# Optimization experiments

Hardware: AMD Instinct MI355X
Metric: run time of the kernel (lower is better)

## Reference

```python
import jax, jax.numpy as jnp
import numpy as np

N_NODES = 200000
N_EDGES = 4000000  # doubled (w2b + b2w), matches edge_weight param size
N_W2B = 2000000


def gcn_conv(x, W, b, src, dst, ew, n):
    # PyG GCNConv with add_self_loops=True, symmetric normalization.
    loop = jnp.arange(n)
    src_sl = jnp.concatenate([src, loop])
    dst_sl = jnp.concatenate([dst, loop])
    w_sl = jnp.concatenate([ew, jnp.ones((n,), ew.dtype)])  # self-loop weight 1
    deg = jax.ops.segment_sum(w_sl, dst_sl, num_segments=n)
    dinv = jnp.where(deg > 0, jax.lax.rsqrt(deg), 0.0)
    norm = dinv[src_sl] * w_sl * dinv[dst_sl]          # [E+N]
    xw = x @ W                                          # [N, out]
    msg = xw[src_sl] * norm[:, None]                    # [E+N, out]
    out = jax.ops.segment_sum(msg, dst_sl, num_segments=n)
    return out + b


def setup_inputs() -> dict:
    key = jax.random.key(0)
    ks = jax.random.split(key, 16)
    h1, h2, h3, h4, out = 8, 16, 32, 4, 3
    inp = 7

    def lin_init(k, fan_in, fan_out):
        bound = 1.0 / np.sqrt(fan_in)
        kw, kb = jax.random.split(k)
        W = jax.random.uniform(kw, (fan_in, fan_out), jnp.float32, -bound, bound)
        b = jax.random.uniform(kb, (fan_out,), jnp.float32, -bound, bound)
        return W, b

    x = jax.random.normal(ks[0], (N_NODES, inp), jnp.float32)
    edge_index = jax.random.randint(ks[1], (2, N_EDGES), 0, N_NODES, jnp.int64)
    w2b = jax.random.randint(ks[2], (2, N_W2B), 0, N_NODES, jnp.int64)
    edge_weight = jnp.ones((N_EDGES,), jnp.float32)  # Parameter init: ones

    W1, b1 = lin_init(ks[3], inp, h1)
    W2, b2 = lin_init(ks[4], h1, h2)
    W3, b3 = lin_init(ks[5], h2, h3)
    Wl1, bl1 = lin_init(ks[6], 2 * h3, h4)
    Wl2, bl2 = lin_init(ks[7], h4, out)

    return dict(x=x, edge_index=edge_index, w2b=w2b, edge_weight=edge_weight,
                W1=W1, b1=b1, W2=W2, b2=b2, W3=W3, b3=b3,
                Wl1=Wl1, bl1=bl1, Wl2=Wl2, bl2=bl2)


def reference(x, edge_index, w2b, edge_weight,
              W1, b1, W2, b2, W3, b3, Wl1, bl1, Wl2, bl2):
    n = x.shape[0]
    src, dst = edge_index[0], edge_index[1]
    ew = jax.nn.sigmoid(edge_weight)
    h = jax.nn.relu(gcn_conv(x, W1, b1, src, dst, ew, n))
    h = jax.nn.relu(gcn_conv(h, W2, b2, src, dst, ew, n))
    h = jax.nn.relu(gcn_conv(h, W3, b3, src, dst, ew, n))
    # fused gather-concat replacing the per-edge python loop
    concat = jnp.concatenate([h[w2b[0]], h[w2b[1]]], axis=-1)  # [E_w2b, 2*h3]
    hidden = concat @ Wl1 + bl1
    edge_pred = hidden @ Wl2 + bl2
    return edge_pred
```

## Files before the change

kernel.cpp:

```cpp
#include <hip/hip_runtime.h>
#include <hip/hip_bf16.h>
#include <hip/hip_fp16.h>


#define NB1 768
#define NPB 256
#define MAXBINS 1024
#define TILE 4096
#define QS 16384.0f
#define QINV (1.0f / 16384.0f)

typedef _Float16 h2 __attribute__((ext_vector_type(2)));
typedef _Float16 h4 __attribute__((ext_vector_type(4)));
typedef _Float16 h8 __attribute__((ext_vector_type(8)));

__device__ __forceinline__ float sigmoidf_(float x) {
    return 1.0f / (1.0f + __expf(-x));
}

__global__ void p1a_hist(const int* __restrict__ dst, int* __restrict__ bh,
                         int ne, int nbins, int chunk) {
    __shared__ int h[MAXBINS];
    for (int k = threadIdx.x; k < nbins; k += 256) h[k] = 0;
    __syncthreads();
    int base = blockIdx.x * chunk;
    int end = min(base + chunk, ne);
    for (int e = base + threadIdx.x; e < end; e += 256)
        atomicAdd(&h[dst[e] >> 8], 1);
    __syncthreads();
    for (int k = threadIdx.x; k < nbins; k += 256)
        bh[(size_t)k * NB1 + blockIdx.x] = h[k];
}

__global__ void s1_scan(int* __restrict__ bh, int* __restrict__ bintot) {
    __shared__ int sums[256];
    constexpr int W = NB1 / 256;
    int* row = bh + (size_t)blockIdx.x * NB1;
    int v[W];
    int s = 0;
#pragma unroll
    for (int j = 0; j < W; ++j) { v[j] = row[threadIdx.x * W + j]; s += v[j]; }
    sums[threadIdx.x] = s;
    __syncthreads();
    for (int o = 1; o < 256; o <<= 1) {
        int t = (threadIdx.x >= o) ? sums[threadIdx.x - o] : 0;
        __syncthreads();
        sums[threadIdx.x] += t;
        __syncthreads();
    }
    int excl = sums[threadIdx.x] - s;
#pragma unroll
    for (int j = 0; j < W; ++j) { row[threadIdx.x * W + j] = excl; excl += v[j]; }
    if (threadIdx.x == 255) bintot[blockIdx.x] = sums[255];
}

__global__ void s2_scan(const int* __restrict__ bintot, int* __restrict__ binbase,
                        int nbins, int ne) {
    __shared__ int tmp[1024];
    int tid = threadIdx.x;
    int v = (tid < nbins) ? bintot[tid] : 0;
    tmp[tid] = v;
    __syncthreads();
    for (int o = 1; o < 1024; o <<= 1) {
        int t = (tid >= o) ? tmp[tid - o] : 0;
        __syncthreads();
        tmp[tid] += t;
        __syncthreads();
    }
    if (tid < nbins) binbase[tid] = tmp[tid] - v;
    if (tid == 0) binbase[nbins] = ne;
}

__global__ void p1b_scatter(const int* __restrict__ src, const int* __restrict__ dst,
                            const float* __restrict__ ew, const int* __restrict__ bh,
                            const int* __restrict__ binbase,
                            unsigned* __restrict__ edlo, unsigned char* __restrict__ eddl,
                            int ne, int nbins, int chunk) {
    __shared__ unsigned slo[TILE];
    __shared__ unsigned shi[TILE];
    __shared__ int hist[MAXBINS];
    __shared__ int boff[MAXBINS];
    __shared__ int cur[MAXBINS];
    __shared__ int wsum[4];
    int tid = threadIdx.x;
    int lane = tid & 63, wid = tid >> 6;
    for (int k = tid; k < nbins; k += 256)
        cur[k] = binbase[k] + bh[(size_t)k * NB1 + blockIdx.x];
    int base = blockIdx.x * chunk;
    int endb = min(base + chunk, ne);
    for (int t0 = base; t0 < endb; t0 += TILE) {
        int cnt = min(TILE, endb - t0);
        for (int k = tid; k < nbins; k += 256) hist[k] = 0;
        __syncthreads();
        for (int j = tid; j < cnt; j += 256)
            atomicAdd(&hist[dst[t0 + j] >> 8], 1);
        __syncthreads();
        int w0 = tid * 4;
        int lv[4];
        int ls = 0;
#pragma unroll
        for (int j = 0; j < 4; ++j) {
            lv[j] = (w0 + j < nbins) ? hist[w0 + j] : 0;
            ls += lv[j];
        }
        int s = ls;
        for (int o = 1; o < 64; o <<= 1) {
            int t = __shfl_up(s, o, 64);
            if (lane >= o) s += t;
        }
        if (lane == 63) wsum[wid] = s;
        __syncthreads();
        int wpre = 0;
        for (int w = 0; w < wid; ++w) wpre += wsum[w];
        int excl = wpre + s - ls;
#pragma unroll
        for (int j = 0; j < 4; ++j) {
            if (w0 + j < nbins) { boff[w0 + j] = excl; excl += lv[j]; }
        }
        __syncthreads();
        for (int j = tid; j < cnt; j += 256) {
            int e = t0 + j;
            int d = dst[e];
            int b = d >> 8;
            float w = sigmoidf_(ew[e]);
            int q = (int)fminf(w * QS + 0.5f, 16383.0f);
            unsigned lo = (unsigned)src[e] | ((unsigned)q << 18);
            int p = atomicAdd(&boff[b], 1);
            slo[p] = lo;
            shi[p] = ((unsigned)b << 8) | (unsigned)(d & 255);
        }
        __syncthreads();
        for (int j = tid; j < cnt; j += 256) {
            unsigned hv = shi[j];
            int b = (int)(hv >> 8);
            int g = cur[b] + (j - (boff[b] - hist[b]));
            edlo[g] = slo[j];
            eddl[g] = (unsigned char)(hv & 255u);
        }
        __syncthreads();
        for (int k = tid; k < nbins; k += 256) cur[k] += hist[k];
        __syncthreads();
    }
}

__global__ void p2_build(const unsigned* __restrict__ edlo, const unsigned char* __restrict__ eddl,
                         const int* __restrict__ binbase, unsigned* __restrict__ edata,
                         int* __restrict__ C, float* __restrict__ dinv,
                         const float* __restrict__ x, const float* __restrict__ W1,
                         _Float16* __restrict__ g0, int n, int ne, int nbins) {
    __shared__ int cnt[NPB];
    __shared__ int curs[NPB];
    __shared__ unsigned qsum[NPB];
    __shared__ float Ws[56];
    __shared__ int wsum[4];
    if (threadIdx.x < 56) Ws[threadIdx.x] = W1[threadIdx.x];
    int b = blockIdx.x;
    int E0 = binbase[b], E1 = binbase[b + 1];
    int tid = threadIdx.x;
    int lane = tid & 63, wid = tid >> 6;
    cnt[tid] = 0;
    qsum[tid] = 0;
    __syncthreads();
    for (int k = E0 + tid; k < E1; k += 256)
        atomicAdd(&cnt[(int)eddl[k]], 1);
    __syncthreads();
    int v = cnt[tid];
    int s = v;
    for (int o = 1; o < 64; o <<= 1) {
        int t = __shfl_up(s, o, 64);
        if (lane >= o) s += t;
    }
    if (lane == 63) wsum[wid] = s;
    __syncthreads();
    int wpre = 0;
    for (int w = 0; w < wid; ++w) wpre += wsum[w];
    int excl = wpre + s - v;
    curs[tid] = E0 + excl;
    int node = b * NPB + tid;
    if (node < n) C[node] = E0 + excl;
    if (b == 0 && tid == 0) C[n] = ne;
    __syncthreads();
    for (int k = E0 + tid; k < E1; k += 256) {
        unsigned lo = edlo[k];
        int dl = (int)eddl[k];
        int pos = atomicAdd(&curs[dl], 1);
        edata[pos] = lo;
        atomicAdd(&qsum[dl], lo >> 18);
    }
    __syncthreads();
    if (node < n) {
        float dv = rsqrtf((float)qsum[tid] * QINV + 1.0f);
        dinv[node] = dv;
        float xi[7];
#pragma unroll
        for (int k = 0; k < 7; ++k) xi[k] = x[(size_t)node * 7 + k];
        h8 r;
#pragma unroll
        for (int o = 0; o < 8; ++o) {
            float acc = 0.0f;
#pragma unroll
            for (int k = 0; k < 7; ++k) acc = fmaf(xi[k], Ws[k * 8 + o], acc);
            r[o] = (_Float16)(acc * dv);
        }
        *reinterpret_cast<h8*>(g0 + (size_t)node * 8) = r;
    }
}

__global__ void gather1_kernel(const _Float16* __restrict__ g, const float* __restrict__ dinv,
                               const int* __restrict__ C, const unsigned* __restrict__ edata,
                               const float* __restrict__ b1, _Float16* __restrict__ out, int n) {
    __shared__ float bs[8];
    if (threadIdx.x < 8) bs[threadIdx.x] = b1[threadIdx.x];
    __syncthreads();
    long long t = (long long)blockIdx.x * blockDim.x + threadIdx.x;
    int i = (int)(t >> 3);
    int l8 = (int)(t & 7);
    if (i >= n) return;
    int beg = C[i], end = C[i + 1];
    float acc[8] = {0.f, 0.f, 0.f, 0.f, 0.f, 0.f, 0.f, 0.f};
    if (l8 == 0) {
        h8 r = *reinterpret_cast<const h8*>(g + (size_t)i * 8);
#pragma unroll
        for (int j = 0; j < 8; ++j) acc[j] = (float)r[j];
    }
    int k = beg + l8;
    for (; k + 8 < end; k += 16) {
        unsigned v0 = edata[k];
        unsigned v1 = edata[k + 8];
        h8 r0 = *reinterpret_cast<const h8*>(g + (size_t)(v0 & 0x3FFFFu) * 8);
        h8 r1 = *reinterpret_cast<const h8*>(g + (size_t)(v1 & 0x3FFFFu) * 8);
        float w0 = (float)(v0 >> 18) * QINV;
        float w1 = (float)(v1 >> 18) * QINV;
#pragma unroll
        for (int j = 0; j < 8; ++j) acc[j] = fmaf((float)r0[j], w0, acc[j]);
#pragma unroll
        for (int j = 0; j < 8; ++j) acc[j] = fmaf((float)r1[j], w1, acc[j]);
    }
    if (k < end) {
        unsigned v = edata[k];
        float w = (float)(v >> 18) * QINV;
        h8 r = *reinterpret_cast<const h8*>(g + (size_t)(v & 0x3FFFFu) * 8);
#pragma unroll
        for (int j = 0; j < 8; ++j) acc[j] = fmaf((float)r[j], w, acc[j]);
    }
    bool t4 = (l8 & 4) != 0, t2 = (l8 & 2) != 0, t1 = (l8 & 1) != 0;
    float s4[4];
#pragma unroll
    for (int j = 0; j < 4; ++j) {
        float keep = t4 ? acc[4 + j] : acc[j];
        float send = t4 ? acc[j] : acc[4 + j];
        s4[j] = keep + __shfl_xor(send, 4, 64);
    }
    float s2[2];
#pragma unroll
    for (int j = 0; j < 2; ++j) {
        float keep = t2 ? s4[2 + j] : s4[j];
        float send = t2 ? s4[j] : s4[2 + j];
        s2[j] = keep + __shfl_xor(send, 2, 64);
    }
    float keep = t1 ? s2[1] : s2[0];
    float send = t1 ? s2[0] : s2[1];
    float s = keep + __shfl_xor(send, 1, 64);
    float dv = dinv[i];
    out[(size_t)i * 8 + l8] = (_Float16)(dv * fmaxf(dv * s + bs[l8], 0.0f));
}

__global__ void gather2_kernel(const _Float16* __restrict__ g, const float* __restrict__ dinv,
                               const int* __restrict__ C, const unsigned* __restrict__ edata,
                               const float* __restrict__ W2, const float* __restrict__ b2,
                               _Float16* __restrict__ out, int n) {
    __shared__ float Ws[128];
    __shared__ float bs[16];
    if (threadIdx.x < 128) Ws[threadIdx.x] = W2[threadIdx.x];
    if (threadIdx.x < 16) bs[threadIdx.x] = b2[threadIdx.x];
    __syncthreads();
    long long t = (long long)blockIdx.x * blockDim.x + threadIdx.x;
    int i = (int)(t >> 3);
    int l8 = (int)(t & 7);
    if (i >= n) return;
    int beg = C[i], end = C[i + 1];
    float acc[8] = {0.f, 0.f, 0.f, 0.f, 0.f, 0.f, 0.f, 0.f};
    if (l8 == 0) {
        h8 r = *reinterpret_cast<const h8*>(g + (size_t)i * 8);
#pragma unroll
        for (int j = 0; j < 8; ++j) acc[j] = (float)r[j];
    }
    int k = beg + l8;
    for (; k + 8 < end; k += 16) {
        unsigned v0 = edata[k];
        unsigned v1 = edata[k + 8];
        h8 r0 = *reinterpret_cast<const h8*>(g + (size_t)(v0 & 0x3FFFFu) * 8);
        h8 r1 = *reinterpret_cast<const h8*>(g + (size_t)(v1 & 0x3FFFFu) * 8);
        float w0 = (float)(v0 >> 18) * QINV;
        float w1 = (float)(v1 >> 18) * QINV;
#pragma unroll
        for (int j = 0; j < 8; ++j) acc[j] = fmaf((float)r0[j], w0, acc[j]);
#pragma unroll
        for (int j = 0; j < 8; ++j) acc[j] = fmaf((float)r1[j], w1, acc[j]);
    }
    if (k < end) {
        unsigned v = edata[k];
        float w = (float)(v >> 18) * QINV;
        h8 r = *reinterpret_cast<const h8*>(g + (size_t)(v & 0x3FFFFu) * 8);
#pragma unroll
        for (int j = 0; j < 8; ++j) acc[j] = fmaf((float)r[j], w, acc[j]);
    }
#pragma unroll
    for (int j = 0; j < 8; ++j) {
        acc[j] += __shfl_xor(acc[j], 1, 64);
        acc[j] += __shfl_xor(acc[j], 2, 64);
        acc[j] += __shfl_xor(acc[j], 4, 64);
    }
    float dv = dinv[i];
    float raw[8];
#pragma unroll
    for (int j = 0; j < 8; ++j) raw[j] = acc[j] * dv;
    int o0 = l8 * 2;
    h2 o2;
#pragma unroll
    for (int jo = 0; jo < 2; ++jo) {
        int o = o0 + jo;
        float h = bs[o];
#pragma unroll
        for (int k2 = 0; k2 < 8; ++k2) h = fmaf(raw[k2], Ws[k2 * 16 + o], h);
        o2[jo] = (_Float16)(dv * fmaxf(h, 0.0f));
    }
    *reinterpret_cast<h2*>(out + (size_t)i * 16 + o0) = o2;
}

__global__ void gather3_kernel(const _Float16* __restrict__ g, const float* __restrict__ dinv,
                               const int* __restrict__ C, const unsigned* __restrict__ edata,
                               _Float16* __restrict__ raw3, int n) {
    long long t = (long long)blockIdx.x * blockDim.x + threadIdx.x;
    int i = (int)(t >> 3);
    int l8 = (int)(t & 7);
    if (i >= n) return;
    int beg = C[i], end = C[i + 1];
    float acc[16];
#pragma unroll
    for (int j = 0; j < 16; ++j) acc[j] = 0.0f;
    if (l8 == 0) {
        h8 r0 = *reinterpret_cast<const h8*>(g + (size_t)i * 16);
        h8 r1 = *reinterpret_cast<const h8*>(g + (size_t)i * 16 + 8);
#pragma unroll
        for (int j = 0; j < 8; ++j) { acc[j] = (float)r0[j]; acc[8 + j] = (float)r1[j]; }
    }
    int k = beg + l8;
    for (; k + 8 < end; k += 16) {
        unsigned v0 = edata[k];
        unsigned v1 = edata[k + 8];
        size_t i0 = (size_t)(v0 & 0x3FFFFu) * 16;
        size_t i1 = (size_t)(v1 & 0x3FFFFu) * 16;
        h8 a0 = *reinterpret_cast<const h8*>(g + i0);
        h8 a1 = *reinterpret_cast<const h8*>(g + i0 + 8);
        h8 c0 = *reinterpret_cast<const h8*>(g + i1);
        h8 c1 = *reinterpret_cast<const h8*>(g + i1 + 8);
        float w0 = (float)(v0 >> 18) * QINV;
        float w1 = (float)(v1 >> 18) * QINV;
#pragma unroll
        for (int j = 0; j < 8; ++j) acc[j] = fmaf((float)a0[j], w0, acc[j]);
#pragma unroll
        for (int j = 0; j < 8; ++j) acc[8 + j] = fmaf((float)a1[j], w0, acc[8 + j]);
#pragma unroll
        for (int j = 0; j < 8; ++j) acc[j] = fmaf((float)c0[j], w1, acc[j]);
#pragma unroll
        for (int j = 0; j < 8; ++j) acc[8 + j] = fmaf((float)c1[j], w1, acc[8 + j]);
    }
    if (k < end) {
        unsigned v = edata[k];
        size_t i0 = (size_t)(v & 0x3FFFFu) * 16;
        h8 a0 = *reinterpret_cast<const h8*>(g + i0);
        h8 a1 = *reinterpret_cast<const h8*>(g + i0 + 8);
        float w = (float)(v >> 18) * QINV;
#pragma unroll
        for (int j = 0; j < 8; ++j) acc[j] = fmaf((float)a0[j], w, acc[j]);
#pragma unroll
        for (int j = 0; j < 8; ++j) acc[8 + j] = fmaf((float)a1[j], w, acc[8 + j]);
    }
    bool t4 = (l8 & 4) != 0, t2 = (l8 & 2) != 0, t1 = (l8 & 1) != 0;
    float s8[8];
#pragma unroll
    for (int j = 0; j < 8; ++j) {
        float keep = t4 ? acc[8 + j] : acc[j];
        float send = t4 ? acc[j] : acc[8 + j];
        s8[j] = keep + __shfl_xor(send, 4, 64);
    }
    float s4[4];
#pragma unroll
    for (int j = 0; j < 4; ++j) {
        float keep = t2 ? s8[4 + j] : s8[j];
        float send = t2 ? s8[j] : s8[4 + j];
        s4[j] = keep + __shfl_xor(send, 2, 64);
    }
    float s2[2];
#pragma unroll
    for (int j = 0; j < 2; ++j) {
        float keep = t1 ? s4[2 + j] : s4[j];
        float send = t1 ? s4[j] : s4[2 + j];
        s2[j] = keep + __shfl_xor(send, 1, 64);
    }
    float dv = dinv[i];
    h2 o2;
    o2[0] = (_Float16)(s2[0] * dv);
    o2[1] = (_Float16)(s2[1] * dv);
    *reinterpret_cast<h2*>(raw3 + (size_t)i * 16 + l8 * 2) = o2;
}

__global__ void dense3_kernel(const _Float16* __restrict__ raw3,
                              const float* __restrict__ W3, const float* __restrict__ b3,
                              const float* __restrict__ Wl1, const float* __restrict__ bl1,
                              const float* __restrict__ Wl2, const float* __restrict__ bl2,
                              _Float16* __restrict__ pqh, int n) {
    __shared__ __align__(16) float WsT[512];
    __shared__ float bs[32];
    __shared__ float wfs[192];
    __shared__ float bfs[3];
    for (int t = threadIdx.x; t < 512; t += 256) {
        int k = t >> 5, o = t & 31;
        WsT[o * 16 + k] = W3[t];
    }
    if (threadIdx.x < 32) bs[threadIdx.x] = b3[threadIdx.x];
    if (threadIdx.x < 192) {
        int f = threadIdx.x / 3, j = threadIdx.x % 3;
        float a = 0.0f;
#pragma unroll
        for (int k = 0; k < 4; ++k) a = fmaf(Wl1[f * 4 + k], Wl2[k * 3 + j], a);
        wfs[threadIdx.x] = a;
    }
    if (threadIdx.x < 3) {
        float a = bl2[threadIdx.x];
#pragma unroll
        for (int k = 0; k < 4; ++k) a = fmaf(bl1[k], Wl2[k * 3 + threadIdx.x], a);
        bfs[threadIdx.x] = a;
    }
    __syncthreads();
    int i = blockIdx.x * 256 + threadIdx.x;
    if (i >= n) return;
    h8 r0 = *reinterpret_cast<const h8*>(raw3 + (size_t)i * 16);
    h8 r1 = *reinterpret_cast<const h8*>(raw3 + (size_t)i * 16 + 8);
    float raw[16];
#pragma unroll
    for (int j = 0; j < 8; ++j) { raw[j] = (float)r0[j]; raw[8 + j] = (float)r1[j]; }
    float p0 = bfs[0], p1 = bfs[1], p2 = bfs[2];
    float q0 = 0.0f, q1 = 0.0f, q2 = 0.0f;
#pragma unroll
    for (int o = 0; o < 32; ++o) {
        const float4* w4 = reinterpret_cast<const float4*>(WsT + o * 16);
        float4 wa = w4[0], wb = w4[1], wc = w4[2], wd = w4[3];
        float h = bs[o];
        h = fmaf(raw[0], wa.x, h);  h = fmaf(raw[1], wa.y, h);
        h = fmaf(raw[2], wa.z, h);  h = fmaf(raw[3], wa.w, h);
        h = fmaf(raw[4], wb.x, h);  h = fmaf(raw[5], wb.y, h);
        h = fmaf(raw[6], wb.z, h);  h = fmaf(raw[7], wb.w, h);
        h = fmaf(raw[8], wc.x, h);  h = fmaf(raw[9], wc.y, h);
        h = fmaf(raw[10], wc.z, h); h = fmaf(raw[11], wc.w, h);
        h = fmaf(raw[12], wd.x, h); h = fmaf(raw[13], wd.y, h);
        h = fmaf(raw[14], wd.z, h); h = fmaf(raw[15], wd.w, h);
        h = fmaxf(h, 0.0f);
        p0 = fmaf(h, wfs[o * 3 + 0], p0);
        p1 = fmaf(h, wfs[o * 3 + 1], p1);
        p2 = fmaf(h, wfs[o * 3 + 2], p2);
        q0 = fmaf(h, wfs[(32 + o) * 3 + 0], q0);
        q1 = fmaf(h, wfs[(32 + o) * 3 + 1], q1);
        q2 = fmaf(h, wfs[(32 + o) * 3 + 2], q2);
    }
    h8 o8;
    o8[0] = (_Float16)p0; o8[1] = (_Float16)p1; o8[2] = (_Float16)p2; o8[3] = (_Float16)0.0f;
    o8[4] = (_Float16)q0; o8[5] = (_Float16)q1; o8[6] = (_Float16)q2; o8[7] = (_Float16)0.0f;
    *reinterpret_cast<h8*>(pqh + (size_t)i * 8) = o8;
}

__global__ void head_kernel(const int* __restrict__ w2b, const _Float16* __restrict__ pqh,
                            float* __restrict__ out, int nw) {
    int e = blockIdx.x * blockDim.x + threadIdx.x;
    if (e >= nw) return;
    int a = w2b[e];
    int b = w2b[(size_t)nw + e];
    h4 P = *reinterpret_cast<const h4*>(pqh + (size_t)a * 8);
    h4 Q = *reinterpret_cast<const h4*>(pqh + (size_t)b * 8 + 4);
    out[(size_t)e * 3 + 0] = (float)P[0] + (float)Q[0];
    out[(size_t)e * 3 + 1] = (float)P[1] + (float)Q[1];
    out[(size_t)e * 3 + 2] = (float)P[2] + (float)Q[2];
}

extern "C" void kernel_launch(void* const* d_in, const int* in_sizes, int n_in,
                              void* d_out, int out_size, void* d_ws, size_t ws_size,
                              hipStream_t stream) {
    const float* x   = (const float*)d_in[0];
    const int* eidx  = (const int*)d_in[1];
    const int* w2b   = (const int*)d_in[2];
    const float* ew  = (const float*)d_in[3];
    const float* W1  = (const float*)d_in[4];
    const float* b1  = (const float*)d_in[5];
    const float* W2  = (const float*)d_in[6];
    const float* b2  = (const float*)d_in[7];
    const float* W3  = (const float*)d_in[8];
    const float* b3  = (const float*)d_in[9];
    const float* Wl1 = (const float*)d_in[10];
    const float* bl1 = (const float*)d_in[11];
    const float* Wl2 = (const float*)d_in[12];
    const float* bl2 = (const float*)d_in[13];
    float* out = (float*)d_out;

    const int n  = in_sizes[0] / 7;
    const int ne = in_sizes[1] / 2;
    const int nw = in_sizes[2] / 2;
    const int* src = eidx;
    const int* dst = eidx + ne;

    const int nbins = (n + NPB - 1) / NPB;
    const int chunk = (ne + NB1 - 1) / NB1;

    float*     ws      = (float*)d_ws;
    float*     dinv    = ws;
    int*       C       = (int*)(ws + n);
    unsigned*  edata   = (unsigned*)(ws + 2 * (size_t)n + 16);
    int*       bh      = (int*)(edata + ne);
    int*       bintot  = bh + (size_t)nbins * NB1;
    int*       binbase = bintot + MAXBINS;
    _Float16*  g0      = (_Float16*)(binbase + MAXBINS);
    float*     bregion = (float*)(g0 + (size_t)n * 8);
    unsigned*  edlo    = (unsigned*)bregion;
    unsigned char* eddl = (unsigned char*)(edlo + ne);
    _Float16*  g1      = (_Float16*)bregion;
    _Float16*  g2      = (_Float16*)(bregion + 4 * (size_t)n);
    _Float16*  pqh     = (_Float16*)(bregion + 12 * (size_t)n);
    _Float16*  raw3    = (_Float16*)(bregion + 16 * (size_t)n);

    const int Bl = 256;
    auto blks = [&](long long t) { return (int)((t + Bl - 1) / Bl); };
    const int nb8 = blks((long long)n * 8);

    p1a_hist<<<NB1, Bl, 0, stream>>>(dst, bh, ne, nbins, chunk);
    s1_scan<<<nbins, Bl, 0, stream>>>(bh, bintot);
    s2_scan<<<1, 1024, 0, stream>>>(bintot, binbase, nbins, ne);
    p1b_scatter<<<NB1, Bl, 0, stream>>>(src, dst, ew, bh, binbase, edlo, eddl, ne, nbins, chunk);
    p2_build<<<nbins, Bl, 0, stream>>>(edlo, eddl, binbase, edata, C, dinv, x, W1, g0, n, ne, nbins);

    gather1_kernel<<<nb8, Bl, 0, stream>>>(g0, dinv, C, edata, b1, g1, n);
    gather2_kernel<<<nb8, Bl, 0, stream>>>(g1, dinv, C, edata, W2, b2, g2, n);
    gather3_kernel<<<nb8, Bl, 0, stream>>>(g2, dinv, C, edata, raw3, n);
    dense3_kernel<<<blks(n), Bl, 0, stream>>>(raw3, W3, b3, Wl1, bl1, Wl2, bl2, pqh, n);

    head_kernel<<<blks(nw), Bl, 0, stream>>>(w2b, pqh, out, nw);
}
```

Measured before the change: 365.0 us.

## Pack binned edges into 64-bit records and use 4 lanes per node in gathers

The binning scatter now reads src, dst and edge weight once per edge and keeps the packed record in registers between the histogram and the local sort. It writes one 64-bit record per edge instead of separate 32-bit and byte arrays, and p2_build reads that single array. The three gather kernels now assign 4 lanes per node instead of 8, which cuts shuffle reduction steps and widens the output stores. The cost is fewer edges in flight per node, so high-degree nodes may see longer serial loops and gather latency may be less well hidden. Shared staging size is unchanged, but register use in the scatter kernel rises.

```diff
diff --git a/kernel.cpp b/kernel.cpp
--- a/kernel.cpp
+++ b/kernel.cpp
@@ -74,14 +74,14 @@
 __global__ void p1b_scatter(const int* __restrict__ src, const int* __restrict__ dst,
                             const float* __restrict__ ew, const int* __restrict__ bh,
                             const int* __restrict__ binbase,
-                            unsigned* __restrict__ edlo, unsigned char* __restrict__ eddl,
+                            unsigned long long* __restrict__ b64,
                             int ne, int nbins, int chunk) {
-    __shared__ unsigned slo[TILE];
-    __shared__ unsigned shi[TILE];
+    __shared__ unsigned long long stage[TILE];
     __shared__ int hist[MAXBINS];
     __shared__ int boff[MAXBINS];
     __shared__ int cur[MAXBINS];
     __shared__ int wsum[4];
+    constexpr int MPT = TILE / 256;
     int tid = threadIdx.x;
     int lane = tid & 63, wid = tid >> 6;
     for (int k = tid; k < nbins; k += 256)
@@ -92,8 +92,19 @@
         int cnt = min(TILE, endb - t0);
         for (int k = tid; k < nbins; k += 256) hist[k] = 0;
         __syncthreads();
-        for (int j = tid; j < cnt; j += 256)
-            atomicAdd(&hist[dst[t0 + j] >> 8], 1);
+        unsigned long long ent[MPT];
+        int m = 0;
+        for (int j = tid; j < cnt; j += 256) {
+            int e = t0 + j;
+            int d = dst[e];
+            float w = sigmoidf_(ew[e]);
+            int q = (int)fminf(w * QS + 0.5f, 16383.0f);
+            int b = d >> 8;
+            ent[m++] = (unsigned long long)((unsigned)src[e] | ((unsigned)q << 18))
+                     | ((unsigned long long)(d & 255) << 32)
+                     | ((unsigned long long)b << 40);
+            atomicAdd(&hist[b], 1);
+        }
         __syncthreads();
         int w0 = tid * 4;
         int lv[4];
@@ -118,24 +129,16 @@
             if (w0 + j < nbins) { boff[w0 + j] = excl; excl += lv[j]; }
         }
         __syncthreads();
+        for (int j = 0; j < m; ++j) {
+            int b = (int)(ent[j] >> 40);
+            int p = atomicAdd(&boff[b], 1);
+            stage[p] = ent[j];
+        }
+        __syncthreads();
         for (int j = tid; j < cnt; j += 256) {
-            int e = t0 + j;
-            int d = dst[e];
-            int b = d >> 8;
-            float w = sigmoidf_(ew[e]);
-            int q = (int)fminf(w * QS + 0.5f, 16383.0f);
-            unsigned lo = (unsigned)src[e] | ((unsigned)q << 18);
-            int p = atomicAdd(&boff[b], 1);
-            slo[p] = lo;
-            shi[p] = ((unsigned)b << 8) | (unsigned)(d & 255);
-        }
-        __syncthreads();
-        for (int j = tid; j < cnt; j += 256) {
-            unsigned hv = shi[j];
-            int b = (int)(hv >> 8);
-            int g = cur[b] + (j - (boff[b] - hist[b]));
-            edlo[g] = slo[j];
-            eddl[g] = (unsigned char)(hv & 255u);
+            unsigned long long v = stage[j];
+            int b = (int)(v >> 40);
+            b64[cur[b] + (j - (boff[b] - hist[b]))] = v;
         }
         __syncthreads();
         for (int k = tid; k < nbins; k += 256) cur[k] += hist[k];
@@ -143,7 +146,7 @@
     }
 }
 
-__global__ void p2_build(const unsigned* __restrict__ edlo, const unsigned char* __restrict__ eddl,
+__global__ void p2_build(const unsigned long long* __restrict__ b64,
                          const int* __restrict__ binbase, unsigned* __restrict__ edata,
                          int* __restrict__ C, float* __restrict__ dinv,
                          const float* __restrict__ x, const float* __restrict__ W1,
@@ -162,7 +165,7 @@
     qsum[tid] = 0;
     __syncthreads();
     for (int k = E0 + tid; k < E1; k += 256)
-        atomicAdd(&cnt[(int)eddl[k]], 1);
+        atomicAdd(&cnt[(int)((b64[k] >> 32) & 0xFF)], 1);
     __syncthreads();
     int v = cnt[tid];
     int s = v;
@@ -181,11 +184,11 @@
     if (b == 0 && tid == 0) C[n] = ne;
     __syncthreads();
     for (int k = E0 + tid; k < E1; k += 256) {
-        unsigned lo = edlo[k];
-        int dl = (int)eddl[k];
+        unsigned long long e64 = b64[k];
+        int dl = (int)((e64 >> 32) & 0xFF);
         int pos = atomicAdd(&curs[dl], 1);
-        edata[pos] = lo;
-        atomicAdd(&qsum[dl], lo >> 18);
+        edata[pos] = (unsigned)(e64 & 0xFFFFFFFFu);
+        atomicAdd(&qsum[dl], (unsigned)((e64 >> 18) & 0x3FFFu));
     }
     __syncthreads();
     if (node < n) {
@@ -213,20 +216,20 @@
     if (threadIdx.x < 8) bs[threadIdx.x] = b1[threadIdx.x];
     __syncthreads();
     long long t = (long long)blockIdx.x * blockDim.x + threadIdx.x;
-    int i = (int)(t >> 3);
-    int l8 = (int)(t & 7);
+    int i = (int)(t >> 2);
+    int l4 = (int)(t & 3);
     if (i >= n) return;
     int beg = C[i], end = C[i + 1];
     float acc[8] = {0.f, 0.f, 0.f, 0.f, 0.f, 0.f, 0.f, 0.f};
-    if (l8 == 0) {
+    if (l4 == 0) {
         h8 r = *reinterpret_cast<const h8*>(g + (size_t)i * 8);
 #pragma unroll
         for (int j = 0; j < 8; ++j) acc[j] = (float)r[j];
     }
-    int k = beg + l8;
-    for (; k + 8 < end; k += 16) {
+    int k = beg + l4;
+    for (; k + 4 < end; k += 8) {
         unsigned v0 = edata[k];
-        unsigned v1 = edata[k + 8];
+        unsigned v1 = edata[k + 4];
         h8 r0 = *reinterpret_cast<const h8*>(g + (size_t)(v0 & 0x3FFFFu) * 8);
         h8 r1 = *reinterpret_cast<const h8*>(g + (size_t)(v1 & 0x3FFFFu) * 8);
         float w0 = (float)(v0 >> 18) * QINV;
@@ -243,26 +246,26 @@
 #pragma unroll
         for (int j = 0; j < 8; ++j) acc[j] = fmaf((float)r[j], w, acc[j]);
     }
-    bool t4 = (l8 & 4) != 0, t2 = (l8 & 2) != 0, t1 = (l8 & 1) != 0;
+    bool f2 = (l4 & 2) != 0, f1 = (l4 & 1) != 0;
     float s4[4];
 #pragma unroll
     for (int j = 0; j < 4; ++j) {
-        float keep = t4 ? acc[4 + j] : acc[j];
-        float send = t4 ? acc[j] : acc[4 + j];
-        s4[j] = keep + __shfl_xor(send, 4, 64);
+        float keep = f2 ? acc[4 + j] : acc[j];
+        float send = f2 ? acc[j] : acc[4 + j];
+        s4[j] = keep + __shfl_xor(send, 2, 64);
     }
     float s2[2];
 #pragma unroll
     for (int j = 0; j < 2; ++j) {
-        float keep = t2 ? s4[2 + j] : s4[j];
-        float send = t2 ? s4[j] : s4[2 + j];
-        s2[j] = keep + __shfl_xor(send, 2, 64);
-    }
-    float keep = t1 ? s2[1] : s2[0];
-    float send = t1 ? s2[0] : s2[1];
-    float s = keep + __shfl_xor(send, 1, 64);
+        float keep = f1 ? s4[2 + j] : s4[j];
+        float send = f1 ? s4[j] : s4[2 + j];
+        s2[j] = keep + __shfl_xor(send, 1, 64);
+    }
     float dv = dinv[i];
-    out[(size_t)i * 8 + l8] = (_Float16)(dv * fmaxf(dv * s + bs[l8], 0.0f));
+    h2 o2;
+    o2[0] = (_Float16)(dv * fmaxf(dv * s2[0] + bs[2 * l4 + 0], 0.0f));
+    o2[1] = (_Float16)(dv * fmaxf(dv * s2[1] + bs[2 * l4 + 1], 0.0f));
+    *reinterpret_cast<h2*>(out + (size_t)i * 8 + 2 * l4) = o2;
 }
 
 __global__ void gather2_kernel(const _Float16* __restrict__ g, const float* __restrict__ dinv,
@@ -275,20 +278,20 @@
     if (threadIdx.x < 16) bs[threadIdx.x] = b2[threadIdx.x];
     __syncthreads();
     long long t = (long long)blockIdx.x * blockDim.x + threadIdx.x;
-    int i = (int)(t >> 3);
-    int l8 = (int)(t & 7);
+    int i = (int)(t >> 2);
+    int l4 = (int)(t & 3);
     if (i >= n) return;
     int beg = C[i], end = C[i + 1];
     float acc[8] = {0.f, 0.f, 0.f, 0.f, 0.f, 0.f, 0.f, 0.f};
-    if (l8 == 0) {
+    if (l4 == 0) {
         h8 r = *reinterpret_cast<const h8*>(g + (size_t)i * 8);
 #pragma unroll
         for (int j = 0; j < 8; ++j) acc[j] = (float)r[j];
     }
-    int k = beg + l8;
-    for (; k + 8 < end; k += 16) {
+    int k = beg + l4;
+    for (; k + 4 < end; k += 8) {
         unsigned v0 = edata[k];
-        unsigned v1 = edata[k + 8];
+        unsigned v1 = edata[k + 4];
         h8 r0 = *reinterpret_cast<const h8*>(g + (size_t)(v0 & 0x3FFFFu) * 8);
         h8 r1 = *reinterpret_cast<const h8*>(g + (size_t)(v1 & 0x3FFFFu) * 8);
         float w0 = (float)(v0 >> 18) * QINV;
@@ -309,46 +312,45 @@
     for (int j = 0; j < 8; ++j) {
         acc[j] += __shfl_xor(acc[j], 1, 64);
         acc[j] += __shfl_xor(acc[j], 2, 64);
-        acc[j] += __shfl_xor(acc[j], 4, 64);
     }
     float dv = dinv[i];
     float raw[8];
 #pragma unroll
     for (int j = 0; j < 8; ++j) raw[j] = acc[j] * dv;
-    int o0 = l8 * 2;
-    h2 o2;
-#pragma unroll
-    for (int jo = 0; jo < 2; ++jo) {
+    int o0 = l4 * 4;
+    h4 o4;
+#pragma unroll
+    for (int jo = 0; jo < 4; ++jo) {
         int o = o0 + jo;
         float h = bs[o];
 #pragma unroll
         for (int k2 = 0; k2 < 8; ++k2) h = fmaf(raw[k2], Ws[k2 * 16 + o], h);
-        o2[jo] = (_Float16)(dv * fmaxf(h, 0.0f));
-    }
-    *reinterpret_cast<h2*>(out + (size_t)i * 16 + o0) = o2;
+        o4[jo] = (_Float16)(dv * fmaxf(h, 0.0f));
+    }
+    *reinterpret_cast<h4*>(out + (size_t)i * 16 + o0) = o4;
 }
 
 __global__ void gather3_kernel(const _Float16* __restrict__ g, const float* __restrict__ dinv,
                                const int* __restrict__ C, const unsigned* __restrict__ edata,
                                _Float16* __restrict__ raw3, int n) {
     long long t = (long long)blockIdx.x * blockDim.x + threadIdx.x;
-    int i = (int)(t >> 3);
-    int l8 = (int)(t & 7);
+    int i = (int)(t >> 2);
+    int l4 = (int)(t & 3);
     if (i >= n) return;
     int beg = C[i], end = C[i + 1];
     float acc[16];
 #pragma unroll
     for (int j = 0; j < 16; ++j) acc[j] = 0.0f;
-    if (l8 == 0) {
+    if (l4 == 0) {
         h8 r0 = *reinterpret_cast<const h8*>(g + (size_t)i * 16);
         h8 r1 = *reinterpret_cast<const h8*>(g + (size_t)i * 16 + 8);
 #pragma unroll
         for (int j = 0; j < 8; ++j) { acc[j] = (float)r0[j]; acc[8 + j] = (float)r1[j]; }
     }
-    int k = beg + l8;
-    for (; k + 8 < end; k += 16) {
+    int k = beg + l4;
+    for (; k + 4 < end; k += 8) {
         unsigned v0 = edata[k];
-        unsigned v1 = edata[k + 8];
+        unsigned v1 = edata[k + 4];
         size_t i0 = (size_t)(v0 & 0x3FFFFu) * 16;
         size_t i1 = (size_t)(v1 & 0x3FFFFu) * 16;
         h8 a0 = *reinterpret_cast<const h8*>(g + i0);
@@ -377,33 +379,26 @@
 #pragma unroll
         for (int j = 0; j < 8; ++j) acc[8 + j] = fmaf((float)a1[j], w, acc[8 + j]);
     }
-    bool t4 = (l8 & 4) != 0, t2 = (l8 & 2) != 0, t1 = (l8 & 1) != 0;
+    bool f2 = (l4 & 2) != 0, f1 = (l4 & 1) != 0;
     float s8[8];
 #pragma unroll
     for (int j = 0; j < 8; ++j) {
-        float keep = t4 ? acc[8 + j] : acc[j];
-        float send = t4 ? acc[j] : acc[8 + j];
-        s8[j] = keep + __shfl_xor(send, 4, 64);
+        float keep = f2 ? acc[8 + j] : acc[j];
+        float send = f2 ? acc[j] : acc[8 + j];
+        s8[j] = keep + __shfl_xor(send, 2, 64);
     }
     float s4[4];
 #pragma unroll
     for (int j = 0; j < 4; ++j) {
-        float keep = t2 ? s8[4 + j] : s8[j];
-        float send = t2 ? s8[j] : s8[4 + j];
-        s4[j] = keep + __shfl_xor(send, 2, 64);
-    }
-    float s2[2];
-#pragma unroll
-    for (int j = 0; j < 2; ++j) {
-        float keep = t1 ? s4[2 + j] : s4[j];
-        float send = t1 ? s4[j] : s4[2 + j];
-        s2[j] = keep + __shfl_xor(send, 1, 64);
+        float keep = f1 ? s8[4 + j] : s8[j];
+        float send = f1 ? s8[j] : s8[4 + j];
+        s4[j] = keep + __shfl_xor(send, 1, 64);
     }
     float dv = dinv[i];
-    h2 o2;
-    o2[0] = (_Float16)(s2[0] * dv);
-    o2[1] = (_Float16)(s2[1] * dv);
-    *reinterpret_cast<h2*>(raw3 + (size_t)i * 16 + l8 * 2) = o2;
+    h4 o4;
+#pragma unroll
+    for (int j = 0; j < 4; ++j) o4[j] = (_Float16)(s4[j] * dv);
+    *reinterpret_cast<h4*>(raw3 + (size_t)i * 16 + 4 * l4) = o4;
 }
 
 __global__ void dense3_kernel(const _Float16* __restrict__ raw3,
@@ -520,8 +515,7 @@
     int*       binbase = bintot + MAXBINS;
     _Float16*  g0      = (_Float16*)(binbase + MAXBINS);
     float*     bregion = (float*)(g0 + (size_t)n * 8);
-    unsigned*  edlo    = (unsigned*)bregion;
-    unsigned char* eddl = (unsigned char*)(edlo + ne);
+    unsigned long long* b64 = (unsigned long long*)bregion;
     _Float16*  g1      = (_Float16*)bregion;
     _Float16*  g2      = (_Float16*)(bregion + 4 * (size_t)n);
     _Float16*  pqh     = (_Float16*)(bregion + 12 * (size_t)n);
@@ -529,17 +523,17 @@
 
     const int Bl = 256;
     auto blks = [&](long long t) { return (int)((t + Bl - 1) / Bl); };
-    const int nb8 = blks((long long)n * 8);
+    const int nb4 = blks((long long)n * 4);
 
     p1a_hist<<<NB1, Bl, 0, stream>>>(dst, bh, ne, nbins, chunk);
     s1_scan<<<nbins, Bl, 0, stream>>>(bh, bintot);
     s2_scan<<<1, 1024, 0, stream>>>(bintot, binbase, nbins, ne);
-    p1b_scatter<<<NB1, Bl, 0, stream>>>(src, dst, ew, bh, binbase, edlo, eddl, ne, nbins, chunk);
-    p2_build<<<nbins, Bl, 0, stream>>>(edlo, eddl, binbase, edata, C, dinv, x, W1, g0, n, ne, nbins);
-
-    gather1_kernel<<<nb8, Bl, 0, stream>>>(g0, dinv, C, edata, b1, g1, n);
-    gather2_kernel<<<nb8, Bl, 0, stream>>>(g1, dinv, C, edata, W2, b2, g2, n);
-    gather3_kernel<<<nb8, Bl, 0, stream>>>(g2, dinv, C, edata, raw3, n);
+    p1b_scatter<<<NB1, Bl, 0, stream>>>(src, dst, ew, bh, binbase, b64, ne, nbins, chunk);
+    p2_build<<<nbins, Bl, 0, stream>>>(b64, binbase, edata, C, dinv, x, W1, g0, n, ne, nbins);
+
+    gather1_kernel<<<nb4, Bl, 0, stream>>>(g0, dinv, C, edata, b1, g1, n);
+    gather2_kernel<<<nb4, Bl, 0, stream>>>(g1, dinv, C, edata, W2, b2, g2, n);
+    gather3_kernel<<<nb4, Bl, 0, stream>>>(g2, dinv, C, edata, raw3, n);
     dense3_kernel<<<blks(n), Bl, 0, stream>>>(raw3, W3, b3, Wl1, bl1, Wl2, bl2, pqh, n);
 
     head_kernel<<<blks(nw), Bl, 0, stream>>>(w2b, pqh, out, nw);
```

Result: faster. 357.7 us (-2.0%).

## Pack scatter entries into 64-bit words and use nontemporal streaming loads

Applied to the files above, without the earlier changes.

The scatter pass now reads dst/src/ew once per tile into registers, packs src, quantized weight, local dst and bin into one 64-bit entry, and stages it through a single shared array. p2_build reads that packed array in place of separate 32-bit and byte arrays. Streaming index and output accesses across the gather and head kernels now use nontemporal loads and stores. This cuts repeated global reads of dst and the uncoalesced byte writes, but adds register pressure for the per-thread entry buffer and more bytes written per edge.

```diff
diff --git a/kernel.cpp b/kernel.cpp
--- a/kernel.cpp
+++ b/kernel.cpp
@@ -26,7 +26,7 @@
     int base = blockIdx.x * chunk;
     int end = min(base + chunk, ne);
     for (int e = base + threadIdx.x; e < end; e += 256)
-        atomicAdd(&h[dst[e] >> 8], 1);
+        atomicAdd(&h[__builtin_nontemporal_load(dst + e) >> 8], 1);
     __syncthreads();
     for (int k = threadIdx.x; k < nbins; k += 256)
         bh[(size_t)k * NB1 + blockIdx.x] = h[k];
@@ -74,14 +74,14 @@
 __global__ void p1b_scatter(const int* __restrict__ src, const int* __restrict__ dst,
                             const float* __restrict__ ew, const int* __restrict__ bh,
                             const int* __restrict__ binbase,
-                            unsigned* __restrict__ edlo, unsigned char* __restrict__ eddl,
+                            unsigned long long* __restrict__ b64,
                             int ne, int nbins, int chunk) {
-    __shared__ unsigned slo[TILE];
-    __shared__ unsigned shi[TILE];
+    __shared__ unsigned long long stage[TILE];
     __shared__ int hist[MAXBINS];
     __shared__ int boff[MAXBINS];
     __shared__ int cur[MAXBINS];
     __shared__ int wsum[4];
+    constexpr int MPT = TILE / 256;
     int tid = threadIdx.x;
     int lane = tid & 63, wid = tid >> 6;
     for (int k = tid; k < nbins; k += 256)
@@ -92,8 +92,20 @@
         int cnt = min(TILE, endb - t0);
         for (int k = tid; k < nbins; k += 256) hist[k] = 0;
         __syncthreads();
-        for (int j = tid; j < cnt; j += 256)
-            atomicAdd(&hist[dst[t0 + j] >> 8], 1);
+        unsigned long long ent[MPT];
+        int m = 0;
+        for (int j = tid; j < cnt; j += 256) {
+            int e = t0 + j;
+            int d = __builtin_nontemporal_load(dst + e);
+            float w = sigmoidf_(__builtin_nontemporal_load(ew + e));
+            int q = (int)fminf(w * QS + 0.5f, 16383.0f);
+            int b = d >> 8;
+            ent[m++] = (unsigned long long)((unsigned)__builtin_nontemporal_load(src + e)
+                                            | ((unsigned)q << 18))
+                     | ((unsigned long long)(d & 255) << 32)
+                     | ((unsigned long long)b << 40);
+            atomicAdd(&hist[b], 1);
+        }
         __syncthreads();
         int w0 = tid * 4;
         int lv[4];
@@ -118,24 +130,16 @@
             if (w0 + j < nbins) { boff[w0 + j] = excl; excl += lv[j]; }
         }
         __syncthreads();
+        for (int j = 0; j < m; ++j) {
+            int b = (int)(ent[j] >> 40);
+            int p = atomicAdd(&boff[b], 1);
+            stage[p] = ent[j];
+        }
+        __syncthreads();
         for (int j = tid; j < cnt; j += 256) {
-            int e = t0 + j;
-            int d = dst[e];
-            int b = d >> 8;
-            float w = sigmoidf_(ew[e]);
-            int q = (int)fminf(w * QS + 0.5f, 16383.0f);
-            unsigned lo = (unsigned)src[e] | ((unsigned)q << 18);
-            int p = atomicAdd(&boff[b], 1);
-            slo[p] = lo;
-            shi[p] = ((unsigned)b << 8) | (unsigned)(d & 255);
-        }
-        __syncthreads();
-        for (int j = tid; j < cnt; j += 256) {
-            unsigned hv = shi[j];
-            int b = (int)(hv >> 8);
-            int g = cur[b] + (j - (boff[b] - hist[b]));
-            edlo[g] = slo[j];
-            eddl[g] = (unsigned char)(hv & 255u);
+            unsigned long long v = stage[j];
+            int b = (int)(v >> 40);
+            b64[cur[b] + (j - (boff[b] - hist[b]))] = v;
         }
         __syncthreads();
         for (int k = tid; k < nbins; k += 256) cur[k] += hist[k];
@@ -143,7 +147,7 @@
     }
 }
 
-__global__ void p2_build(const unsigned* __restrict__ edlo, const unsigned char* __restrict__ eddl,
+__global__ void p2_build(const unsigned long long* __restrict__ b64,
                          const int* __restrict__ binbase, unsigned* __restrict__ edata,
                          int* __restrict__ C, float* __restrict__ dinv,
                          const float* __restrict__ x, const float* __restrict__ W1,
@@ -162,7 +166,7 @@
     qsum[tid] = 0;
     __syncthreads();
     for (int k = E0 + tid; k < E1; k += 256)
-        atomicAdd(&cnt[(int)eddl[k]], 1);
+        atomicAdd(&cnt[(int)((__builtin_nontemporal_load(b64 + k) >> 32) & 0xFF)], 1);
     __syncthreads();
     int v = cnt[tid];
     int s = v;
@@ -181,11 +185,11 @@
     if (b == 0 && tid == 0) C[n] = ne;
     __syncthreads();
     for (int k = E0 + tid; k < E1; k += 256) {
-        unsigned lo = edlo[k];
-        int dl = (int)eddl[k];
+        unsigned long long e64 = __builtin_nontemporal_load(b64 + k);
+        int dl = (int)((e64 >> 32) & 0xFF);
         int pos = atomicAdd(&curs[dl], 1);
-        edata[pos] = lo;
-        atomicAdd(&qsum[dl], lo >> 18);
+        edata[pos] = (unsigned)(e64 & 0xFFFFFFFFu);
+        atomicAdd(&qsum[dl], (unsigned)((e64 >> 18) & 0x3FFFu));
     }
     __syncthreads();
     if (node < n) {
@@ -225,8 +229,8 @@
     }
     int k = beg + l8;
     for (; k + 8 < end; k += 16) {
-        unsigned v0 = edata[k];
-        unsigned v1 = edata[k + 8];
+        unsigned v0 = __builtin_nontemporal_load(edata + k);
+        unsigned v1 = __builtin_nontemporal_load(edata + k + 8);
         h8 r0 = *reinterpret_cast<const h8*>(g + (size_t)(v0 & 0x3FFFFu) * 8);
         h8 r1 = *reinterpret_cast<const h8*>(g + (size_t)(v1 & 0x3FFFFu) * 8);
         float w0 = (float)(v0 >> 18) * QINV;
@@ -237,7 +241,7 @@
         for (int j = 0; j < 8; ++j) acc[j] = fmaf((float)r1[j], w1, acc[j]);
     }
     if (k < end) {
-        unsigned v = edata[k];
+        unsigned v = __builtin_nontemporal_load(edata + k);
         float w = (float)(v >> 18) * QINV;
         h8 r = *reinterpret_cast<const h8*>(g + (size_t)(v & 0x3FFFFu) * 8);
 #pragma unroll
@@ -287,8 +291,8 @@
     }
     int k = beg + l8;
     for (; k + 8 < end; k += 16) {
-        unsigned v0 = edata[k];
-        unsigned v1 = edata[k + 8];
+        unsigned v0 = __builtin_nontemporal_load(edata + k);
+        unsigned v1 = __builtin_nontemporal_load(edata + k + 8);
         h8 r0 = *reinterpret_cast<const h8*>(g + (size_t)(v0 & 0x3FFFFu) * 8);
         h8 r1 = *reinterpret_cast<const h8*>(g + (size_t)(v1 & 0x3FFFFu) * 8);
         float w0 = (float)(v0 >> 18) * QINV;
@@ -299,7 +303,7 @@
         for (int j = 0; j < 8; ++j) acc[j] = fmaf((float)r1[j], w1, acc[j]);
     }
     if (k < end) {
-        unsigned v = edata[k];
+        unsigned v = __builtin_nontemporal_load(edata + k);
         float w = (float)(v >> 18) * QINV;
         h8 r = *reinterpret_cast<const h8*>(g + (size_t)(v & 0x3FFFFu) * 8);
 #pragma unroll
@@ -347,8 +351,8 @@
     }
     int k = beg + l8;
     for (; k + 8 < end; k += 16) {
-        unsigned v0 = edata[k];
-        unsigned v1 = edata[k + 8];
+        unsigned v0 = __builtin_nontemporal_load(edata + k);
+        unsigned v1 = __builtin_nontemporal_load(edata + k + 8);
         size_t i0 = (size_t)(v0 & 0x3FFFFu) * 16;
         size_t i1 = (size_t)(v1 & 0x3FFFFu) * 16;
         h8 a0 = *reinterpret_cast<const h8*>(g + i0);
@@ -367,7 +371,7 @@
         for (int j = 0; j < 8; ++j) acc[8 + j] = fmaf((float)c1[j], w1, acc[8 + j]);
     }
     if (k < end) {
-        unsigned v = edata[k];
+        unsigned v = __builtin_nontemporal_load(edata + k);
         size_t i0 = (size_t)(v & 0x3FFFFu) * 16;
         h8 a0 = *reinterpret_cast<const h8*>(g + i0);
         h8 a1 = *reinterpret_cast<const h8*>(g + i0 + 8);
@@ -474,13 +478,13 @@
                             float* __restrict__ out, int nw) {
     int e = blockIdx.x * blockDim.x + threadIdx.x;
     if (e >= nw) return;
-    int a = w2b[e];
-    int b = w2b[(size_t)nw + e];
+    int a = __builtin_nontemporal_load(w2b + e);
+    int b = __builtin_nontemporal_load(w2b + (size_t)nw + e);
     h4 P = *reinterpret_cast<const h4*>(pqh + (size_t)a * 8);
     h4 Q = *reinterpret_cast<const h4*>(pqh + (size_t)b * 8 + 4);
-    out[(size_t)e * 3 + 0] = (float)P[0] + (float)Q[0];
-    out[(size_t)e * 3 + 1] = (float)P[1] + (float)Q[1];
-    out[(size_t)e * 3 + 2] = (float)P[2] + (float)Q[2];
+    __builtin_nontemporal_store((float)P[0] + (float)Q[0], out + (size_t)e * 3 + 0);
+    __builtin_nontemporal_store((float)P[1] + (float)Q[1], out + (size_t)e * 3 + 1);
+    __builtin_nontemporal_store((float)P[2] + (float)Q[2], out + (size_t)e * 3 + 2);
 }
 
 extern "C" void kernel_launch(void* const* d_in, const int* in_sizes, int n_in,
@@ -520,8 +524,7 @@
     int*       binbase = bintot + MAXBINS;
     _Float16*  g0      = (_Float16*)(binbase + MAXBINS);
     float*     bregion = (float*)(g0 + (size_t)n * 8);
-    unsigned*  edlo    = (unsigned*)bregion;
-    unsigned char* eddl = (unsigned char*)(edlo + ne);
+    unsigned long long* b64 = (unsigned long long*)bregion;
     _Float16*  g1      = (_Float16*)bregion;
     _Float16*  g2      = (_Float16*)(bregion + 4 * (size_t)n);
     _Float16*  pqh     = (_Float16*)(bregion + 12 * (size_t)n);
@@ -534,8 +537,8 @@
     p1a_hist<<<NB1, Bl, 0, stream>>>(dst, bh, ne, nbins, chunk);
     s1_scan<<<nbins, Bl, 0, stream>>>(bh, bintot);
     s2_scan<<<1, 1024, 0, stream>>>(bintot, binbase, nbins, ne);
-    p1b_scatter<<<NB1, Bl, 0, stream>>>(src, dst, ew, bh, binbase, edlo, eddl, ne, nbins, chunk);
-    p2_build<<<nbins, Bl, 0, stream>>>(edlo, eddl, binbase, edata, C, dinv, x, W1, g0, n, ne, nbins);
+    p1b_scatter<<<NB1, Bl, 0, stream>>>(src, dst, ew, bh, binbase, b64, ne, nbins, chunk);
+    p2_build<<<nbins, Bl, 0, stream>>>(b64, binbase, edata, C, dinv, x, W1, g0, n, ne, nbins);
 
     gather1_kernel<<<nb8, Bl, 0, stream>>>(g0, dinv, C, edata, b1, g1, n);
     gather2_kernel<<<nb8, Bl, 0, stream>>>(g1, dinv, C, edata, W2, b2, g2, n);
```

Result: no change. 371.3 us (+1.7%).
